# Optimization experiments

Measured on AMD Instinct MI355X. Metric: run time of the kernel, lower is better.

The kernel has to match this reference:

```python
import jax, jax.numpy as jnp
import numpy as np

H = 64       # HIDDEN_DIM
HIST = 4     # HIST_LEN
V = 64       # VOCAB_SIZE
LSTM_H = 32  # trigger LSTM hidden size


def setup_inputs() -> dict:
    key = jax.random.key(0)
    ks = jax.random.split(key, 24)
    B, L, M = 1024, 256, 256
    s = 0.1

    def p(k, shape):
        return jax.random.normal(k, shape, dtype=jnp.float32) * s

    return {
        "seq": jax.random.randint(ks[0], (B, L), 0, V, dtype=jnp.int32),
        "memory": jax.random.normal(ks[1], (B, M, H), dtype=jnp.float32),
        # nn.Embedding(V, H)
        "embed_w": p(ks[2], (V, H)),
        # nn.GRUCell(2H, H): weight_ih (3H, 2H), weight_hh (3H, H)
        "gru_wih": p(ks[3], (3 * H, 2 * H)),
        "gru_whh": p(ks[4], (3 * H, H)),
        "gru_bih": p(ks[5], (3 * H,)),
        "gru_bhh": p(ks[6], (3 * H,)),
        # SoftAttentionMemory projections: Linear(H, H) each
        "q_w": p(ks[7], (H, H)), "q_b": p(ks[8], (H,)),
        "k_w": p(ks[9], (H, H)), "k_b": p(ks[10], (H,)),
        "v_w": p(ks[11], (H, H)), "v_b": p(ks[12], (H,)),
        # PredictiveTrigger nn.LSTM(H, 32): gate order i,f,g,o
        "lstm_wih": p(ks[13], (4 * LSTM_H, H)),
        "lstm_whh": p(ks[14], (4 * LSTM_H, LSTM_H)),
        "lstm_bih": p(ks[15], (4 * LSTM_H,)),
        "lstm_bhh": p(ks[16], (4 * LSTM_H,)),
        "trig_w": p(ks[17], (1, LSTM_H)), "trig_b": p(ks[18], (1,)),
        # output head Linear(H, V)
        "head_w": p(ks[19], (V, H)), "head_b": p(ks[20], (V,)),
    }


def reference(seq, memory, embed_w, gru_wih, gru_whh, gru_bih, gru_bhh,
              q_w, q_b, k_w, k_b, v_w, v_b,
              lstm_wih, lstm_whh, lstm_bih, lstm_bhh,
              trig_w, trig_b, head_w, head_b):
    B, L = seq.shape
    x_emb = embed_w[seq]                         # (B, L, H)
    # k/v projections of memory are time-invariant -> hoist out of the loop
    kmem = memory @ k_w.T + k_b                  # (B, M, H)
    vmem = memory @ v_w.T + v_b                  # (B, M, H)
    scale = 1.0 / jnp.sqrt(jnp.float32(H))

    def gru_cell(inp, h):
        gi = inp @ gru_wih.T + gru_bih           # (B, 3H)
        gh = h @ gru_whh.T + gru_bhh
        i_r, i_z, i_n = jnp.split(gi, 3, axis=-1)
        h_r, h_z, h_n = jnp.split(gh, 3, axis=-1)
        r = jax.nn.sigmoid(i_r + h_r)
        z = jax.nn.sigmoid(i_z + h_z)
        n = jnp.tanh(i_n + r * h_n)
        return (1.0 - z) * n + z * h

    def trigger(hist):                            # hist: (B, HIST, H) -> (B,)
        def lstm_step(carry, x_t):
            hh, cc = carry
            g = x_t @ lstm_wih.T + lstm_bih + hh @ lstm_whh.T + lstm_bhh
            i, f, gg, o = jnp.split(g, 4, axis=-1)
            cc = jax.nn.sigmoid(f) * cc + jax.nn.sigmoid(i) * jnp.tanh(gg)
            hh = jax.nn.sigmoid(o) * jnp.tanh(cc)
            return (hh, cc), None
        init = (jnp.zeros((hist.shape[0], LSTM_H), hist.dtype),
                jnp.zeros((hist.shape[0], LSTM_H), hist.dtype))
        (hh, _), _ = jax.lax.scan(lstm_step, init, jnp.swapaxes(hist, 0, 1))
        return jax.nn.sigmoid(hh @ trig_w.T + trig_b)[:, 0]

    def attend(h):                                # (B, H) -> (B, H)
        q = h @ q_w.T + q_b
        w = jax.nn.softmax(jnp.einsum('bh,bmh->bm', q, kmem) * scale, axis=-1)
        return jnp.einsum('bm,bmh->bh', w, vmem)

    def step(carry, xs):
        h, retrieved, hist, reads = carry
        x_t, t = xs
        h = gru_cell(jnp.concatenate([x_t, retrieved], axis=-1), h)
        # torch uses h.detach() for the trigger history
        hist = jnp.concatenate([hist[:, 1:], jax.lax.stop_gradient(h)[:, None]], axis=1)
        full = t >= HIST - 1                      # history buffer filled
        prob = trigger(hist)
        do_read = full & (jnp.mean(prob) > 0.5)
        retrieved = jnp.where(do_read, attend(h),
                              jnp.where(full, jnp.zeros_like(retrieved), retrieved))
        reads = reads + do_read.astype(jnp.float32)
        return (h, retrieved, hist, reads), None

    carry0 = (jnp.zeros((B, H), jnp.float32),
              jnp.zeros((B, H), jnp.float32),
              jnp.zeros((B, HIST, H), jnp.float32),
              jnp.float32(0.0))
    (h, _, _, reads), _ = jax.lax.scan(step, carry0,
                                       (jnp.swapaxes(x_emb, 0, 1), jnp.arange(L)))
    logits = h @ head_w.T + head_b               # (B, V)
    read_rate = reads / L
    return logits, read_rate
```

## Files before the change

kernel.cpp:

```cpp
#include <hip/hip_runtime.h>
#include <hip/hip_fp16.h>
#include <math.h>

#define OFF_TOKPROJ 0
#define OFF_ACC     12288
#define OFF_SLOT2   12800
#define OFF_SLOTS   78336

#define THRESH30 (512ULL << 30)
#define THRESH27 (512ULL << 27)
#define SPIN_BOUND (1 << 18)

__device__ __forceinline__ float sigf(float x) {
    return __fdividef(1.f, 1.f + __expf(-x));
}
__device__ __forceinline__ float tanhf_fast(float x) {
    float e2 = __expf(-2.f * fabsf(x));
    float r = __fdividef(1.f - e2, 1.f + e2);
    return __uint_as_float(__float_as_uint(r) | (__float_as_uint(x) & 0x80000000u));
}
__device__ __forceinline__ float merged_go(float q, int l) {
    bool lo = (l < 32);
    float e = __expf(lo ? -2.f * fabsf(q) : -q);
    float m = __fdividef(lo ? (1.f - e) : 1.f, 1.f + e);
    if (lo) m = __uint_as_float(__float_as_uint(m) | (__float_as_uint(q) & 0x80000000u));
    return m;
}
__device__ __forceinline__ unsigned int pack2(float x, float y) {
    union { unsigned int u; _Float16 h[2]; } v;
    v.h[0] = (_Float16)x; v.h[1] = (_Float16)y;
    return v.u;
}
__device__ __forceinline__ float unplo(unsigned int u) {
    union { unsigned int x; _Float16 h[2]; } v; v.x = u; return (float)v.h[0];
}
__device__ __forceinline__ float unphi(unsigned int u) {
    union { unsigned int x; _Float16 h[2]; } v; v.x = u; return (float)v.h[1];
}
__device__ __forceinline__ float dot2acc(unsigned int a, unsigned int b, float acc) {
#if __has_builtin(__builtin_amdgcn_fdot2)
    typedef _Float16 hf2 __attribute__((ext_vector_type(2)));
    union { unsigned int u; hf2 h; } ua, ub;
    ua.u = a; ub.u = b;
    return __builtin_amdgcn_fdot2(ua.h, ub.h, acc, false);
#else
    union { unsigned int u; _Float16 h[2]; } ua, ub;
    ua.u = a; ub.u = b;
    return acc + (float)ua.h[0] * (float)ub.h[0] + (float)ua.h[1] * (float)ub.h[1];
#endif
}

__global__ __launch_bounds__(64) void prep_k(
    const float* __restrict__ embed, const float* __restrict__ gwih,
    const float* __restrict__ gbih, float* __restrict__ ws)
{
    int blk = blockIdx.x, l = threadIdx.x;
    if (blk < 64) {
        float* tokproj = ws + OFF_TOKPROJ;
        int v = blk;
        for (int j = l; j < 192; j += 64) {
            float s = gbih[j];
            for (int d = 0; d < 64; ++d) s += embed[v * 64 + d] * gwih[j * 128 + d];
            tokproj[v * 192 + j] = s;
        }
    } else {
        float* z = ws + OFF_SLOT2;
        int base = (blk - 64) * 4096;
        for (int i = base + l; i < base + 4096; i += 64) z[i] = 0.f;
    }
}

__global__ __launch_bounds__(256) void fused_k(
    const int* __restrict__ seq, const float* __restrict__ gwhh,
    const float* __restrict__ gbhh, const float* __restrict__ lwih,
    const float* __restrict__ lwhh, const float* __restrict__ lbih,
    const float* __restrict__ lbhh, const float* __restrict__ tw,
    const float* __restrict__ tb, const float* __restrict__ hw,
    const float* __restrict__ hb, float* __restrict__ ws,
    float* __restrict__ out)
{
    int tid = threadIdx.x, w = tid >> 6, l = tid & 63;
    int r = blockIdx.x;
    int gw = r & 3;
    const float* tokproj = ws + OFF_TOKPROJ;
    unsigned int* slots = (unsigned int*)(ws + OFF_SLOTS);

    __shared__ unsigned int hbuf[2][19][32];
    __shared__ unsigned int hs2w[4][16];
    __shared__ int toks[256];

    for (int i = tid; i < 256; i += 256) toks[i] = seq[(size_t)r * 256 + i];
    __syncthreads();

    if (w == gw) {
        unsigned int wh0h[32], wh1h[32], wh2h[32];
        #pragma unroll
        for (int d2 = 0; d2 < 32; ++d2) {
            wh0h[d2] = pack2(gwhh[(size_t)l * 64 + 2*d2], gwhh[(size_t)l * 64 + 2*d2 + 1]);
            wh1h[d2] = pack2(gwhh[(size_t)(64 + l) * 64 + 2*d2], gwhh[(size_t)(64 + l) * 64 + 2*d2 + 1]);
            wh2h[d2] = pack2(gwhh[(size_t)(128 + l) * 64 + 2*d2], gwhh[(size_t)(128 + l) * 64 + 2*d2 + 1]);
        }
        float g0b = gbhh[l], g1b = gbhh[64 + l], g2b = gbhh[128 + l];
        float h = 0.f;
        if (l < 32) { hbuf[0][0][l] = 0u; hbuf[0][1][l] = 0u; hbuf[0][2][l] = 0u; }
        int tok0 = toks[0];
        float gi0 = tokproj[tok0 * 192 + l], gi1 = tokproj[tok0 * 192 + 64 + l],
              gi2 = tokproj[tok0 * 192 + 128 + l];

        for (int c = 0; c < 16; ++c) {
            int cb = c & 1;
            if (c > 0 && l < 32) {
                hbuf[cb][0][l] = hbuf[cb ^ 1][16][l];
                hbuf[cb][1][l] = hbuf[cb ^ 1][17][l];
                hbuf[cb][2][l] = hbuf[cb ^ 1][18][l];
            }
            for (int s = 0; s < 16; ++s) {
                int t = c * 16 + s;
                float ni0 = 0.f, ni1 = 0.f, ni2 = 0.f;
                if (t < 255) {
                    int tk = toks[t + 1];
                    ni0 = tokproj[tk * 192 + l];
                    ni1 = tokproj[tk * 192 + 64 + l];
                    ni2 = tokproj[tk * 192 + 128 + l];
                }
                float A00 = 0.f, A01 = 0.f, A10 = 0.f, A11 = 0.f, A20 = 0.f, A21 = 0.f;
                #pragma unroll
                for (int d8 = 0; d8 < 8; ++d8) {
                    uint4 hv = *(const uint4*)&hbuf[cb][s + 2][d8 * 4];
                    A00 = dot2acc(hv.x, wh0h[d8*4+0], A00); A01 = dot2acc(hv.y, wh0h[d8*4+1], A01);
                    A00 = dot2acc(hv.z, wh0h[d8*4+2], A00); A01 = dot2acc(hv.w, wh0h[d8*4+3], A01);
                    A10 = dot2acc(hv.x, wh1h[d8*4+0], A10); A11 = dot2acc(hv.y, wh1h[d8*4+1], A11);
                    A10 = dot2acc(hv.z, wh1h[d8*4+2], A10); A11 = dot2acc(hv.w, wh1h[d8*4+3], A11);
                    A20 = dot2acc(hv.x, wh2h[d8*4+0], A20); A21 = dot2acc(hv.y, wh2h[d8*4+1], A21);
                    A20 = dot2acc(hv.z, wh2h[d8*4+2], A20); A21 = dot2acc(hv.w, wh2h[d8*4+3], A21);
                }
                float gh0 = g0b + A00 + A01;
                float gh1 = g1b + A10 + A11;
                float gh2 = g2b + A20 + A21;
                float r_ = sigf(gi0 + gh0), z_ = sigf(gi1 + gh1);
                float n_ = tanhf_fast(gi2 + r_ * gh2);
                h = (1.f - z_) * n_ + z_ * h;
                float a0 = __shfl(h, 2 * l), a1 = __shfl(h, 2 * l + 1);
                if (l < 32) hbuf[cb][s + 3][l] = pack2(a0, a1);
                gi0 = ni0; gi1 = ni1; gi2 = ni2;
            }
            __syncthreads();
        }
        float sL = hb[l];
        #pragma unroll
        for (int d4 = 0; d4 < 16; ++d4) {
            float4 w4 = *(const float4*)(hw + (size_t)l * 64 + d4 * 4);
            unsigned int h0 = hbuf[1][18][d4 * 2], h1 = hbuf[1][18][d4 * 2 + 1];
            sL += unplo(h0) * w4.x + unphi(h0) * w4.y + unplo(h1) * w4.z + unphi(h1) * w4.w;
        }
        out[r * 64 + l] = sL;
    } else {
        int tr = (w - gw + 3) & 3;
        unsigned int wl0h[32], wl1h[32], lh0h[16], lh1h[16];
        #pragma unroll
        for (int d2 = 0; d2 < 32; ++d2) {
            wl0h[d2] = pack2(lwih[(size_t)l * 64 + 2*d2], lwih[(size_t)l * 64 + 2*d2 + 1]);
            wl1h[d2] = pack2(lwih[(size_t)(64 + l) * 64 + 2*d2], lwih[(size_t)(64 + l) * 64 + 2*d2 + 1]);
        }
        #pragma unroll
        for (int d2 = 0; d2 < 16; ++d2) {
            lh0h[d2] = pack2(lwhh[(size_t)l * 32 + 2*d2], lwhh[(size_t)l * 32 + 2*d2 + 1]);
            lh1h[d2] = pack2(lwhh[(size_t)(64 + l) * 32 + 2*d2], lwhh[(size_t)(64 + l) * 32 + 2*d2 + 1]);
        }
        float lb0 = lbih[l] + lbhh[l], lb1 = lbih[64 + l] + lbhh[64 + l];
        float twr = (l < 32) ? tw[l] : 0.f;
        float tb0 = tb[0];

        auto do_chunk = [&](int cc) {
            int bb = cc & 1, base = cc * 16;
            int tlo = (cc == 0) ? 3 : base;
            int n = base + 16 - tlo;
            int ta = tlo + (tr * n) / 3;
            int tb_ = tlo + ((tr + 1) * n) / 3;
            auto proj = [&](int tt) -> unsigned int {
                int idx = tt - base + 3;
                float p0 = lb0, p1 = lb1;
                #pragma unroll
                for (int d8 = 0; d8 < 8; ++d8) {
                    uint4 hv = *(const uint4*)&hbuf[bb][idx][d8 * 4];
                    p0 = dot2acc(hv.x, wl0h[d8*4+0], p0); p1 = dot2acc(hv.x, wl1h[d8*4+0], p1);
                    p0 = dot2acc(hv.y, wl0h[d8*4+1], p0); p1 = dot2acc(hv.y, wl1h[d8*4+1], p1);
                    p0 = dot2acc(hv.z, wl0h[d8*4+2], p0); p1 = dot2acc(hv.z, wl1h[d8*4+2], p1);
                    p0 = dot2acc(hv.w, wl0h[d8*4+3], p0); p1 = dot2acc(hv.w, wl1h[d8*4+3], p1);
                }
                return pack2(p0, p1);
            };
            unsigned int PW[4];
            for (int t = ta; t < tb_; ++t) {
                if (t == ta) {
                    PW[0] = proj(t - 3); PW[1] = proj(t - 2);
                    PW[2] = proj(t - 1); PW[3] = proj(t);
                } else {
                    PW[0] = PW[1]; PW[1] = PW[2]; PW[2] = PW[3];
                    PW[3] = proj(t);
                }
                float hh = 0.f, cc2 = 0.f;
                #pragma unroll
                for (int k = 0; k < 4; ++k) {
                    float q0 = unplo(PW[k]), q1 = unphi(PW[k]);
                    if (k) {
                        #pragma unroll
                        for (int d4 = 0; d4 < 4; ++d4) {
                            uint4 ha = *(const uint4*)&hs2w[w][d4 * 4];
                            q0 = dot2acc(ha.x, lh0h[d4*4+0], q0); q1 = dot2acc(ha.x, lh1h[d4*4+0], q1);
                            q0 = dot2acc(ha.y, lh0h[d4*4+1], q0); q1 = dot2acc(ha.y, lh1h[d4*4+1], q1);
                            q0 = dot2acc(ha.z, lh0h[d4*4+2], q0); q1 = dot2acc(ha.z, lh1h[d4*4+2], q1);
                            q0 = dot2acc(ha.w, lh0h[d4*4+3], q0); q1 = dot2acc(ha.w, lh1h[d4*4+3], q1);
                        }
                    }
                    float s0 = sigf(q0);
                    float m  = merged_go(q1, l);
                    float ff = __shfl(s0, l + 32);
                    float oo = __shfl(m,  l + 32);
                    float ncc = ff * cc2 + s0 * m;
                    float nh = oo * tanhf_fast(ncc);
                    if (l < 32) { cc2 = ncc; hh = nh; }
                    if (k < 3) {
                        float a0 = __shfl(nh, 2 * l), a1 = __shfl(nh, 2 * l + 1);
                        if (l < 16) hs2w[w][l] = pack2(a0, a1);
                    }
                }
                float pp = (l < 32) ? hh * twr : 0.f;
                #pragma unroll
                for (int o = 32; o; o >>= 1) pp += __shfl_xor(pp, o);
                if (l == 0) {
                    float prob = sigf(pp + tb0);
                    unsigned long long q = (unsigned long long)llrint((double)prob * 1073741824.0);
                    if (q > 0x3FFFFFFFull) q = 0x3FFFFFFFull;
                    slots[(size_t)t * 1024 + r] = (unsigned int)q;
                }
            }
        };

        for (int c = 0; c < 16; ++c) {
            if (c > 0) do_chunk(c - 1);
            __syncthreads();
        }
        do_chunk(15);
    }
}

__global__ __launch_bounds__(256) void red_k(float* __restrict__ ws)
{
    int tid = threadIdx.x, w = tid >> 6, l = tid & 63;
    int t = 3 + blockIdx.x * 4 + w;
    if (t > 255) return;
    const unsigned int* slots = (const unsigned int*)(ws + OFF_SLOTS);
    unsigned long long* acc = (unsigned long long*)(ws + OFF_ACC);
    unsigned long long s = 0;
    #pragma unroll
    for (int k = 0; k < 16; ++k) s += slots[(size_t)t * 1024 + k * 64 + l];
    #pragma unroll
    for (int o = 32; o; o >>= 1) s += __shfl_xor(s, o);
    if (l == 0) acc[t] = s;
}

__global__ __launch_bounds__(256, 1) void fin_k(
    const int* __restrict__ seq, const float* __restrict__ memory,
    const float* __restrict__ gwih, const float* __restrict__ gwhh,
    const float* __restrict__ gbhh, const float* __restrict__ qw,
    const float* __restrict__ qb, const float* __restrict__ kw,
    const float* __restrict__ vw, const float* __restrict__ vb,
    const float* __restrict__ lwih, const float* __restrict__ lwhh,
    const float* __restrict__ lbih, const float* __restrict__ lbhh,
    const float* __restrict__ tw, const float* __restrict__ tb,
    const float* __restrict__ hw, const float* __restrict__ hb,
    float* __restrict__ ws, float* __restrict__ out)
{
    int tid = threadIdx.x, w = tid >> 6, l = tid & 63, b = blockIdx.x;
    const unsigned long long* acc = (const unsigned long long*)(ws + OFF_ACC);

    __shared__ int redmin[4];
    {
        int mymin = 1 << 30;
        if (tid >= 3 && acc[tid] > THRESH30) mymin = tid;
        #pragma unroll
        for (int o = 32; o; o >>= 1) mymin = min(mymin, __shfl_xor(mymin, o));
        if (l == 0) redmin[w] = mymin;
    }
    __syncthreads();
    int tc = min(min(redmin[0], redmin[1]), min(redmin[2], redmin[3]));
    if (tc > 255) {
        if (b == 0 && tid == 0) out[65536] = 0.f;
        return;
    }

    int r = b * 4 + w;
    const float* tokproj = ws + OFF_TOKPROJ;
    unsigned int* S2 = (unsigned int*)(ws + OFF_SLOT2);

    __shared__ float hs[4][64], qs[4][64], us[4][64], rs[4][64];
    __shared__ float hs2f[4][32];
    __shared__ float PXl[4][4][128];
    __shared__ unsigned int probq[4];
    __shared__ int flagLds;
    __shared__ int toks[4][256];

    for (int k = 0; k < 4; ++k) toks[w][k * 64 + l] = seq[r * 256 + k * 64 + l];
    if (tid == 0) flagLds = 0;

    float wh0[64], wh1[64], wh2[64], wl0[64], wl1[64], lh0[32], lh1[32];
    #pragma unroll
    for (int d4 = 0; d4 < 16; ++d4) {
        float4 a0 = *(const float4*)(gwhh + (size_t)l * 64 + d4 * 4);
        float4 a1 = *(const float4*)(gwhh + (size_t)(64 + l) * 64 + d4 * 4);
        float4 a2 = *(const float4*)(gwhh + (size_t)(128 + l) * 64 + d4 * 4);
        float4 b0 = *(const float4*)(lwih + (size_t)l * 64 + d4 * 4);
        float4 b1 = *(const float4*)(lwih + (size_t)(64 + l) * 64 + d4 * 4);
        wh0[d4*4] = a0.x; wh0[d4*4+1] = a0.y; wh0[d4*4+2] = a0.z; wh0[d4*4+3] = a0.w;
        wh1[d4*4] = a1.x; wh1[d4*4+1] = a1.y; wh1[d4*4+2] = a1.z; wh1[d4*4+3] = a1.w;
        wh2[d4*4] = a2.x; wh2[d4*4+1] = a2.y; wh2[d4*4+2] = a2.z; wh2[d4*4+3] = a2.w;
        wl0[d4*4] = b0.x; wl0[d4*4+1] = b0.y; wl0[d4*4+2] = b0.z; wl0[d4*4+3] = b0.w;
        wl1[d4*4] = b1.x; wl1[d4*4+1] = b1.y; wl1[d4*4+2] = b1.z; wl1[d4*4+3] = b1.w;
    }
    #pragma unroll
    for (int d4 = 0; d4 < 8; ++d4) {
        float4 c0 = *(const float4*)(lwhh + (size_t)l * 32 + d4 * 4);
        float4 c1 = *(const float4*)(lwhh + (size_t)(64 + l) * 32 + d4 * 4);
        lh0[d4*4] = c0.x; lh0[d4*4+1] = c0.y; lh0[d4*4+2] = c0.z; lh0[d4*4+3] = c0.w;
        lh1[d4*4] = c1.x; lh1[d4*4+1] = c1.y; lh1[d4*4+2] = c1.z; lh1[d4*4+3] = c1.w;
    }
    float g0b = gbhh[l], g1b = gbhh[64 + l], g2b = gbhh[128 + l];
    float lb0 = lbih[l] + lbhh[l], lb1 = lbih[64 + l] + lbhh[64 + l];
    float twr = (l < 32) ? tw[l] : 0.f;
    float tb0 = tb[0];
    const float* mrow = memory + (size_t)r * 16384;

    float h = 0.f;
    hs[w][l] = 0.f;
    bool fire = false, brk = false;
    int cnt = 1;
    __syncthreads();

    for (int t = 0; t < 256; ++t) {
        int tok = toks[w][t];
        float gi0 = tokproj[tok * 192 + l], gi1 = tokproj[tok * 192 + 64 + l],
              gi2 = tokproj[tok * 192 + 128 + l];
        float gh0 = g0b, gh1 = g1b, gh2 = g2b;
        #pragma unroll
        for (int d4 = 0; d4 < 16; ++d4) {
            float4 hv = *(const float4*)&hs[w][d4 * 4];
            gh0 += hv.x*wh0[d4*4] + hv.y*wh0[d4*4+1] + hv.z*wh0[d4*4+2] + hv.w*wh0[d4*4+3];
            gh1 += hv.x*wh1[d4*4] + hv.y*wh1[d4*4+1] + hv.z*wh1[d4*4+2] + hv.w*wh1[d4*4+3];
            gh2 += hv.x*wh2[d4*4] + hv.y*wh2[d4*4+1] + hv.z*wh2[d4*4+2] + hv.w*wh2[d4*4+3];
        }
        if (fire) {
            float q = qb[l];
            #pragma unroll
            for (int d4 = 0; d4 < 16; ++d4) {
                float4 q4 = *(const float4*)(qw + (size_t)l * 64 + d4 * 4);
                float4 hv = *(const float4*)&hs[w][d4 * 4];
                q += hv.x * q4.x + hv.y * q4.y + hv.z * q4.z + hv.w * q4.w;
            }
            qs[w][l] = q;
            float qk = 0.f;
            for (int e = 0; e < 64; ++e) qk += qs[w][e] * kw[(size_t)e * 64 + l];
            qk *= 0.125f;
            us[w][l] = qk;
            float sc[4];
            for (int k = 0; k < 4; ++k) {
                const float* mp = mrow + (size_t)(k * 64 + l) * 64;
                float s = 0.f;
                #pragma unroll
                for (int d4 = 0; d4 < 16; ++d4) {
                    float4 m4 = *(const float4*)(mp + d4 * 4);
                    float4 kv = *(const float4*)&us[w][d4 * 4];
                    s += m4.x * kv.x + m4.y * kv.y + m4.z * kv.z + m4.w * kv.w;
                }
                sc[k] = s;
            }
            float mx = fmaxf(fmaxf(sc[0], sc[1]), fmaxf(sc[2], sc[3]));
            for (int o = 32; o; o >>= 1) mx = fmaxf(mx, __shfl_xor(mx, o));
            float den = 0.f;
            #pragma unroll
            for (int k = 0; k < 4; ++k) { sc[k] = expf(sc[k] - mx); den += sc[k]; }
            for (int o = 32; o; o >>= 1) den += __shfl_xor(den, o);
            float u = 0.f;
            for (int m = 0; m < 256; ++m) {
                float wm = __shfl(sc[m >> 6], m & 63);
                u += wm * mrow[(size_t)m * 64 + l];
            }
            u /= den;
            us[w][l] = u;
            float ret = vb[l];
            #pragma unroll
            for (int d4 = 0; d4 < 16; ++d4) {
                float4 v4 = *(const float4*)(vw + (size_t)l * 64 + d4 * 4);
                float4 uv = *(const float4*)&us[w][d4 * 4];
                ret += uv.x * v4.x + uv.y * v4.y + uv.z * v4.z + uv.w * v4.w;
            }
            rs[w][l] = ret;
            for (int e = 0; e < 64; ++e) {
                float re = rs[w][e];
                gi0 += re * gwih[(size_t)l * 128 + 64 + e];
                gi1 += re * gwih[(size_t)(64 + l) * 128 + 64 + e];
                gi2 += re * gwih[(size_t)(128 + l) * 128 + 64 + e];
            }
        }
        fire = false;
        float r_ = sigf(gi0 + gh0), z_ = sigf(gi1 + gh1);
        float n_ = tanhf_fast(gi2 + r_ * gh2);
        h = (1.f - z_) * n_ + z_ * h;
        hs[w][l] = h;

        float p0 = lb0, p1 = lb1;
        #pragma unroll
        for (int d4 = 0; d4 < 16; ++d4) {
            float4 hv = *(const float4*)&hs[w][d4 * 4];
            p0 += hv.x*wl0[d4*4] + hv.y*wl0[d4*4+1] + hv.z*wl0[d4*4+2] + hv.w*wl0[d4*4+3];
            p1 += hv.x*wl1[d4*4] + hv.y*wl1[d4*4+1] + hv.z*wl1[d4*4+2] + hv.w*wl1[d4*4+3];
        }
        PXl[w][t & 3][l] = p0; PXl[w][t & 3][64 + l] = p1;

        if (t == tc) {
            fire = true;
        } else if (t > tc) {
            float hh = 0.f, cc = 0.f;
            #pragma unroll
            for (int k = 0; k < 4; ++k) {
                int s2 = (t - 3 + k) & 3;
                float q0 = PXl[w][s2][l], q1 = PXl[w][s2][64 + l];
                if (k) {
                    #pragma unroll
                    for (int d4 = 0; d4 < 8; ++d4) {
                        float4 hv = *(const float4*)&hs2f[w][d4 * 4];
                        q0 += hv.x*lh0[d4*4] + hv.y*lh0[d4*4+1] + hv.z*lh0[d4*4+2] + hv.w*lh0[d4*4+3];
                        q1 += hv.x*lh1[d4*4] + hv.y*lh1[d4*4+1] + hv.z*lh1[d4*4+2] + hv.w*lh1[d4*4+3];
                    }
                }
                float f_ = __shfl(q0, l + 32), o_ = __shfl(q1, l + 32);
                float ig = sigf(q0), ff = sigf(f_), gg = tanhf_fast(q1), oo = sigf(o_);
                float ncc = ff * cc + ig * gg;
                float nhh = oo * tanhf_fast(ncc);
                if (l < 32) { cc = ncc; hh = nhh; hs2f[w][l] = nhh; }
            }
            float pp = (l < 32) ? hh * twr : 0.f;
            #pragma unroll
            for (int o = 32; o; o >>= 1) pp += __shfl_xor(pp, o);
            if (l == 0) {
                float prob = sigf(pp + tb0);
                unsigned long long q = (unsigned long long)llrint((double)prob * 134217728.0);
                if (q > 0x7FFFFFFull) q = 0x7FFFFFFull;
                probq[w] = (unsigned int)q;
            }
            __syncthreads();
            if (w == 0 && l == 0) {
                unsigned int s = probq[0] + probq[1] + probq[2] + probq[3];
                __hip_atomic_store(&S2[(size_t)t * 256 + b], (1u << 30) | s,
                                   __ATOMIC_RELAXED, __HIP_MEMORY_SCOPE_AGENT);
            }
            if (w == 0) {
                unsigned long long tot = 0; int spin = 0; bool ok = true;
                if (!brk) {
                    for (;;) {
                        bool all4 = true; tot = 0;
                        #pragma unroll
                        for (int k2 = 0; k2 < 4; ++k2) {
                            unsigned int v = __hip_atomic_load(&S2[(size_t)t * 256 + k2 * 64 + l],
                                                               __ATOMIC_RELAXED, __HIP_MEMORY_SCOPE_AGENT);
                            all4 &= ((v >> 30) == 1u);
                            tot += (v & 0x3FFFFFFFu);
                        }
                        if (__all(all4)) break;
                        if (++spin > SPIN_BOUND) { ok = false; brk = true; break; }
                        __builtin_amdgcn_s_sleep(1);
                    }
                } else ok = false;
                #pragma unroll
                for (int o = 32; o; o >>= 1) tot += __shfl_xor(tot, o);
                int dec = (ok && tot > THRESH27) ? 1 : 0;
                cnt += dec;
                if (l == 0) flagLds = dec;
            }
            __syncthreads();
            fire = (flagLds != 0);
        }
    }

    float sL = hb[l];
    #pragma unroll
    for (int d4 = 0; d4 < 16; ++d4) {
        float4 w4 = *(const float4*)(hw + (size_t)l * 64 + d4 * 4);
        float4 hv = *(const float4*)&hs[w][d4 * 4];
        sL += hv.x * w4.x + hv.y * w4.y + hv.z * w4.z + hv.w * w4.w;
    }
    out[r * 64 + l] = sL;
    if (b == 0 && w == 0 && l == 0)
        out[65536] = brk ? -1234.f : (float)cnt / 256.f;
}

extern "C" void kernel_launch(void* const* d_in, const int* in_sizes, int n_in,
                              void* d_out, int out_size, void* d_ws, size_t ws_size,
                              hipStream_t stream)
{
    const int*   seq    = (const int*)d_in[0];
    const float* memory = (const float*)d_in[1];
    const float* embed  = (const float*)d_in[2];
    const float* gwih   = (const float*)d_in[3];
    const float* gwhh   = (const float*)d_in[4];
    const float* gbih   = (const float*)d_in[5];
    const float* gbhh   = (const float*)d_in[6];
    const float* qw     = (const float*)d_in[7];
    const float* qb     = (const float*)d_in[8];
    const float* kw     = (const float*)d_in[9];
    const float* vw     = (const float*)d_in[11];
    const float* vb     = (const float*)d_in[12];
    const float* lwih   = (const float*)d_in[13];
    const float* lwhh   = (const float*)d_in[14];
    const float* lbih   = (const float*)d_in[15];
    const float* lbhh   = (const float*)d_in[16];
    const float* tw     = (const float*)d_in[17];
    const float* tb     = (const float*)d_in[18];
    const float* hw     = (const float*)d_in[19];
    const float* hb     = (const float*)d_in[20];
    float* ws = (float*)d_ws;
    float* out = (float*)d_out;

    prep_k<<<80, 64, 0, stream>>>(embed, gwih, gbih, ws);
    fused_k<<<1024, 256, 0, stream>>>(seq, gwhh, gbhh, lwih, lwhh, lbih, lbhh,
                                      tw, tb, hw, hb, ws, out);
    red_k<<<64, 256, 0, stream>>>(ws);
    fin_k<<<256, 256, 0, stream>>>(seq, memory, gwih, gwhh, gbhh, qw, qb, kw,
                                   vw, vb, lwih, lwhh, lbih, lbhh, tw, tb,
                                   hw, hb, ws, out);
}
```

Before: 456.6 us.

## Process two batch rows per block in fused GRU/trigger kernel

Each fused_k block now advances two independent sequences, so 512 blocks replace 1024. The GRU warp interleaves the two rows' recurrent dot products to expose ILP and hide the latency of the serial step chain. The three trigger warps split the combined 2×chunk work among themselves. This roughly doubles the per-step work in the GRU warp and its register pressure, and halves the grid, which may lower occupancy and parallelism across CUs.

```diff
diff --git a/kernel.cpp b/kernel.cpp
--- a/kernel.cpp
+++ b/kernel.cpp
@@ -80,16 +80,16 @@
     float* __restrict__ out)
 {
     int tid = threadIdx.x, w = tid >> 6, l = tid & 63;
-    int r = blockIdx.x;
-    int gw = r & 3;
+    int b = blockIdx.x;
+    int gw = b & 3;
     const float* tokproj = ws + OFF_TOKPROJ;
     unsigned int* slots = (unsigned int*)(ws + OFF_SLOTS);
 
-    __shared__ unsigned int hbuf[2][19][32];
+    __shared__ unsigned int hbuf[2][2][19][32];
     __shared__ unsigned int hs2w[4][16];
-    __shared__ int toks[256];
-
-    for (int i = tid; i < 256; i += 256) toks[i] = seq[(size_t)r * 256 + i];
+    __shared__ int toks[2][256];
+
+    for (int i = tid; i < 512; i += 256) toks[i >> 8][i & 255] = seq[(size_t)b * 512 + i];
     __syncthreads();
 
     if (w == gw) {
@@ -101,59 +101,88 @@
             wh2h[d2] = pack2(gwhh[(size_t)(128 + l) * 64 + 2*d2], gwhh[(size_t)(128 + l) * 64 + 2*d2 + 1]);
         }
         float g0b = gbhh[l], g1b = gbhh[64 + l], g2b = gbhh[128 + l];
-        float h = 0.f;
-        if (l < 32) { hbuf[0][0][l] = 0u; hbuf[0][1][l] = 0u; hbuf[0][2][l] = 0u; }
-        int tok0 = toks[0];
-        float gi0 = tokproj[tok0 * 192 + l], gi1 = tokproj[tok0 * 192 + 64 + l],
-              gi2 = tokproj[tok0 * 192 + 128 + l];
+        float h0 = 0.f, h1 = 0.f;
+        if (l < 32) {
+            hbuf[0][0][0][l] = 0u; hbuf[0][0][1][l] = 0u; hbuf[0][0][2][l] = 0u;
+            hbuf[1][0][0][l] = 0u; hbuf[1][0][1][l] = 0u; hbuf[1][0][2][l] = 0u;
+        }
+        int ta = toks[0][0], tbk = toks[1][0];
+        float ga0 = tokproj[ta * 192 + l], ga1 = tokproj[ta * 192 + 64 + l],
+              ga2 = tokproj[ta * 192 + 128 + l];
+        float gb0 = tokproj[tbk * 192 + l], gb1 = tokproj[tbk * 192 + 64 + l],
+              gb2 = tokproj[tbk * 192 + 128 + l];
 
         for (int c = 0; c < 16; ++c) {
             int cb = c & 1;
             if (c > 0 && l < 32) {
-                hbuf[cb][0][l] = hbuf[cb ^ 1][16][l];
-                hbuf[cb][1][l] = hbuf[cb ^ 1][17][l];
-                hbuf[cb][2][l] = hbuf[cb ^ 1][18][l];
+                hbuf[0][cb][0][l] = hbuf[0][cb ^ 1][16][l];
+                hbuf[0][cb][1][l] = hbuf[0][cb ^ 1][17][l];
+                hbuf[0][cb][2][l] = hbuf[0][cb ^ 1][18][l];
+                hbuf[1][cb][0][l] = hbuf[1][cb ^ 1][16][l];
+                hbuf[1][cb][1][l] = hbuf[1][cb ^ 1][17][l];
+                hbuf[1][cb][2][l] = hbuf[1][cb ^ 1][18][l];
             }
             for (int s = 0; s < 16; ++s) {
                 int t = c * 16 + s;
-                float ni0 = 0.f, ni1 = 0.f, ni2 = 0.f;
+                float na0 = 0.f, na1 = 0.f, na2 = 0.f, nb0 = 0.f, nb1 = 0.f, nb2 = 0.f;
                 if (t < 255) {
-                    int tk = toks[t + 1];
-                    ni0 = tokproj[tk * 192 + l];
-                    ni1 = tokproj[tk * 192 + 64 + l];
-                    ni2 = tokproj[tk * 192 + 128 + l];
+                    int tk0 = toks[0][t + 1], tk1 = toks[1][t + 1];
+                    na0 = tokproj[tk0 * 192 + l];
+                    na1 = tokproj[tk0 * 192 + 64 + l];
+                    na2 = tokproj[tk0 * 192 + 128 + l];
+                    nb0 = tokproj[tk1 * 192 + l];
+                    nb1 = tokproj[tk1 * 192 + 64 + l];
+                    nb2 = tokproj[tk1 * 192 + 128 + l];
                 }
-                float A00 = 0.f, A01 = 0.f, A10 = 0.f, A11 = 0.f, A20 = 0.f, A21 = 0.f;
+                float A00=0.f, A01=0.f, A10=0.f, A11=0.f, A20=0.f, A21=0.f;
+                float B00=0.f, B01=0.f, B10=0.f, B11=0.f, B20=0.f, B21=0.f;
                 #pragma unroll
                 for (int d8 = 0; d8 < 8; ++d8) {
-                    uint4 hv = *(const uint4*)&hbuf[cb][s + 2][d8 * 4];
-                    A00 = dot2acc(hv.x, wh0h[d8*4+0], A00); A01 = dot2acc(hv.y, wh0h[d8*4+1], A01);
-                    A00 = dot2acc(hv.z, wh0h[d8*4+2], A00); A01 = dot2acc(hv.w, wh0h[d8*4+3], A01);
-                    A10 = dot2acc(hv.x, wh1h[d8*4+0], A10); A11 = dot2acc(hv.y, wh1h[d8*4+1], A11);
-                    A10 = dot2acc(hv.z, wh1h[d8*4+2], A10); A11 = dot2acc(hv.w, wh1h[d8*4+3], A11);
-                    A20 = dot2acc(hv.x, wh2h[d8*4+0], A20); A21 = dot2acc(hv.y, wh2h[d8*4+1], A21);
-                    A20 = dot2acc(hv.z, wh2h[d8*4+2], A20); A21 = dot2acc(hv.w, wh2h[d8*4+3], A21);
+                    uint4 hv0 = *(const uint4*)&hbuf[0][cb][s + 2][d8 * 4];
+                    uint4 hv1 = *(const uint4*)&hbuf[1][cb][s + 2][d8 * 4];
+                    A00 = dot2acc(hv0.x, wh0h[d8*4+0], A00); A01 = dot2acc(hv0.y, wh0h[d8*4+1], A01);
+                    B00 = dot2acc(hv1.x, wh0h[d8*4+0], B00); B01 = dot2acc(hv1.y, wh0h[d8*4+1], B01);
+                    A00 = dot2acc(hv0.z, wh0h[d8*4+2], A00); A01 = dot2acc(hv0.w, wh0h[d8*4+3], A01);
+                    B00 = dot2acc(hv1.z, wh0h[d8*4+2], B00); B01 = dot2acc(hv1.w, wh0h[d8*4+3], B01);
+                    A10 = dot2acc(hv0.x, wh1h[d8*4+0], A10); A11 = dot2acc(hv0.y, wh1h[d8*4+1], A11);
+                    B10 = dot2acc(hv1.x, wh1h[d8*4+0], B10); B11 = dot2acc(hv1.y, wh1h[d8*4+1], B11);
+                    A10 = dot2acc(hv0.z, wh1h[d8*4+2], A10); A11 = dot2acc(hv0.w, wh1h[d8*4+3], A11);
+                    B10 = dot2acc(hv1.z, wh1h[d8*4+2], B10); B11 = dot2acc(hv1.w, wh1h[d8*4+3], B11);
+                    A20 = dot2acc(hv0.x, wh2h[d8*4+0], A20); A21 = dot2acc(hv0.y, wh2h[d8*4+1], A21);
+                    B20 = dot2acc(hv1.x, wh2h[d8*4+0], B20); B21 = dot2acc(hv1.y, wh2h[d8*4+1], B21);
+                    A20 = dot2acc(hv0.z, wh2h[d8*4+2], A20); A21 = dot2acc(hv0.w, wh2h[d8*4+3], A21);
+                    B20 = dot2acc(hv1.z, wh2h[d8*4+2], B20); B21 = dot2acc(hv1.w, wh2h[d8*4+3], B21);
                 }
-                float gh0 = g0b + A00 + A01;
-                float gh1 = g1b + A10 + A11;
-                float gh2 = g2b + A20 + A21;
-                float r_ = sigf(gi0 + gh0), z_ = sigf(gi1 + gh1);
-                float n_ = tanhf_fast(gi2 + r_ * gh2);
-                h = (1.f - z_) * n_ + z_ * h;
-                float a0 = __shfl(h, 2 * l), a1 = __shfl(h, 2 * l + 1);
-                if (l < 32) hbuf[cb][s + 3][l] = pack2(a0, a1);
-                gi0 = ni0; gi1 = ni1; gi2 = ni2;
+                float r0_ = sigf(ga0 + g0b + A00 + A01);
+                float r1_ = sigf(gb0 + g0b + B00 + B01);
+                float z0_ = sigf(ga1 + g1b + A10 + A11);
+                float z1_ = sigf(gb1 + g1b + B10 + B11);
+                float n0_ = tanhf_fast(ga2 + r0_ * (g2b + A20 + A21));
+                float n1_ = tanhf_fast(gb2 + r1_ * (g2b + B20 + B21));
+                h0 = (1.f - z0_) * n0_ + z0_ * h0;
+                h1 = (1.f - z1_) * n1_ + z1_ * h1;
+                float a0 = __shfl(h0, 2 * l), a1 = __shfl(h0, 2 * l + 1);
+                float b0 = __shfl(h1, 2 * l), b1 = __shfl(h1, 2 * l + 1);
+                if (l < 32) {
+                    hbuf[0][cb][s + 3][l] = pack2(a0, a1);
+                    hbuf[1][cb][s + 3][l] = pack2(b0, b1);
+                }
+                ga0 = na0; ga1 = na1; ga2 = na2;
+                gb0 = nb0; gb1 = nb1; gb2 = nb2;
             }
             __syncthreads();
         }
-        float sL = hb[l];
-        #pragma unroll
-        for (int d4 = 0; d4 < 16; ++d4) {
-            float4 w4 = *(const float4*)(hw + (size_t)l * 64 + d4 * 4);
-            unsigned int h0 = hbuf[1][18][d4 * 2], h1 = hbuf[1][18][d4 * 2 + 1];
-            sL += unplo(h0) * w4.x + unphi(h0) * w4.y + unplo(h1) * w4.z + unphi(h1) * w4.w;
-        }
-        out[r * 64 + l] = sL;
+        #pragma unroll
+        for (int row = 0; row < 2; ++row) {
+            float sL = hb[l];
+            #pragma unroll
+            for (int d4 = 0; d4 < 16; ++d4) {
+                float4 w4 = *(const float4*)(hw + (size_t)l * 64 + d4 * 4);
+                unsigned int q0 = hbuf[row][1][18][d4 * 2], q1 = hbuf[row][1][18][d4 * 2 + 1];
+                sL += unplo(q0) * w4.x + unphi(q0) * w4.y + unplo(q1) * w4.z + unphi(q1) * w4.w;
+            }
+            out[(size_t)(b * 2 + row) * 64 + l] = sL;
+        }
     } else {
         int tr = (w - gw + 3) & 3;
         unsigned int wl0h[32], wl1h[32], lh0h[16], lh1h[16];
@@ -175,65 +204,72 @@
             int bb = cc & 1, base = cc * 16;
             int tlo = (cc == 0) ? 3 : base;
             int n = base + 16 - tlo;
-            int ta = tlo + (tr * n) / 3;
-            int tb_ = tlo + ((tr + 1) * n) / 3;
-            auto proj = [&](int tt) -> unsigned int {
-                int idx = tt - base + 3;
-                float p0 = lb0, p1 = lb1;
-                #pragma unroll
-                for (int d8 = 0; d8 < 8; ++d8) {
-                    uint4 hv = *(const uint4*)&hbuf[bb][idx][d8 * 4];
-                    p0 = dot2acc(hv.x, wl0h[d8*4+0], p0); p1 = dot2acc(hv.x, wl1h[d8*4+0], p1);
-                    p0 = dot2acc(hv.y, wl0h[d8*4+1], p0); p1 = dot2acc(hv.y, wl1h[d8*4+1], p1);
-                    p0 = dot2acc(hv.z, wl0h[d8*4+2], p0); p1 = dot2acc(hv.z, wl1h[d8*4+2], p1);
-                    p0 = dot2acc(hv.w, wl0h[d8*4+3], p0); p1 = dot2acc(hv.w, wl1h[d8*4+3], p1);
-                }
-                return pack2(p0, p1);
-            };
-            unsigned int PW[4];
-            for (int t = ta; t < tb_; ++t) {
-                if (t == ta) {
-                    PW[0] = proj(t - 3); PW[1] = proj(t - 2);
-                    PW[2] = proj(t - 1); PW[3] = proj(t);
-                } else {
-                    PW[0] = PW[1]; PW[1] = PW[2]; PW[2] = PW[3];
-                    PW[3] = proj(t);
-                }
-                float hh = 0.f, cc2 = 0.f;
-                #pragma unroll
-                for (int k = 0; k < 4; ++k) {
-                    float q0 = unplo(PW[k]), q1 = unphi(PW[k]);
-                    if (k) {
-                        #pragma unroll
-                        for (int d4 = 0; d4 < 4; ++d4) {
-                            uint4 ha = *(const uint4*)&hs2w[w][d4 * 4];
-                            q0 = dot2acc(ha.x, lh0h[d4*4+0], q0); q1 = dot2acc(ha.x, lh1h[d4*4+0], q1);
-                            q0 = dot2acc(ha.y, lh0h[d4*4+1], q0); q1 = dot2acc(ha.y, lh1h[d4*4+1], q1);
-                            q0 = dot2acc(ha.z, lh0h[d4*4+2], q0); q1 = dot2acc(ha.z, lh1h[d4*4+2], q1);
-                            q0 = dot2acc(ha.w, lh0h[d4*4+3], q0); q1 = dot2acc(ha.w, lh1h[d4*4+3], q1);
+            int total = 2 * n;
+            int i0 = (tr * total) / 3, i1 = ((tr + 1) * total) / 3;
+            int i = i0;
+            while (i < i1) {
+                int row = i / n;
+                int tstart = tlo + (i - row * n);
+                int iend = min(i1, (row + 1) * n);
+                int tend = tlo + (iend - row * n);
+                auto proj = [&](int tt) -> unsigned int {
+                    int idx = tt - base + 3;
+                    float p0 = lb0, p1 = lb1;
+                    #pragma unroll
+                    for (int d8 = 0; d8 < 8; ++d8) {
+                        uint4 hv = *(const uint4*)&hbuf[row][bb][idx][d8 * 4];
+                        p0 = dot2acc(hv.x, wl0h[d8*4+0], p0); p1 = dot2acc(hv.x, wl1h[d8*4+0], p1);
+                        p0 = dot2acc(hv.y, wl0h[d8*4+1], p0); p1 = dot2acc(hv.y, wl1h[d8*4+1], p1);
+                        p0 = dot2acc(hv.z, wl0h[d8*4+2], p0); p1 = dot2acc(hv.z, wl1h[d8*4+2], p1);
+                        p0 = dot2acc(hv.w, wl0h[d8*4+3], p0); p1 = dot2acc(hv.w, wl1h[d8*4+3], p1);
+                    }
+                    return pack2(p0, p1);
+                };
+                unsigned int PW[4];
+                PW[0] = proj(tstart - 3); PW[1] = proj(tstart - 2);
+                PW[2] = proj(tstart - 1); PW[3] = proj(tstart);
+                for (int t = tstart; t < tend; ++t) {
+                    if (t > tstart) {
+                        PW[0] = PW[1]; PW[1] = PW[2]; PW[2] = PW[3];
+                        PW[3] = proj(t);
+                    }
+                    float hh = 0.f, cc2 = 0.f;
+                    #pragma unroll
+                    for (int k = 0; k < 4; ++k) {
+                        float q0 = unplo(PW[k]), q1 = unphi(PW[k]);
+                        if (k) {
+                            #pragma unroll
+                            for (int d4 = 0; d4 < 4; ++d4) {
+                                uint4 ha = *(const uint4*)&hs2w[w][d4 * 4];
+                                q0 = dot2acc(ha.x, lh0h[d4*4+0], q0); q1 = dot2acc(ha.x, lh1h[d4*4+0], q1);
+                                q0 = dot2acc(ha.y, lh0h[d4*4+1], q0); q1 = dot2acc(ha.y, lh1h[d4*4+1], q1);
+                                q0 = dot2acc(ha.z, lh0h[d4*4+2], q0); q1 = dot2acc(ha.z, lh1h[d4*4+2], q1);
+                                q0 = dot2acc(ha.w, lh0h[d4*4+3], q0); q1 = dot2acc(ha.w, lh1h[d4*4+3], q1);
+                            }
+                        }
+                        float s0 = sigf(q0);
+                        float m  = merged_go(q1, l);
+                        float ff = __shfl(s0, l + 32);
+                        float oo = __shfl(m,  l + 32);
+                        float ncc = ff * cc2 + s0 * m;
+                        float nh = oo * tanhf_fast(ncc);
+                        if (l < 32) { cc2 = ncc; hh = nh; }
+                        if (k < 3) {
+                            float a0 = __shfl(nh, 2 * l), a1 = __shfl(nh, 2 * l + 1);
+                            if (l < 16) hs2w[w][l] = pack2(a0, a1);
                         }
                     }
-                    float s0 = sigf(q0);
-                    float m  = merged_go(q1, l);
-                    float ff = __shfl(s0, l + 32);
-                    float oo = __shfl(m,  l + 32);
-                    float ncc = ff * cc2 + s0 * m;
-                    float nh = oo * tanhf_fast(ncc);
-                    if (l < 32) { cc2 = ncc; hh = nh; }
-                    if (k < 3) {
-                        float a0 = __shfl(nh, 2 * l), a1 = __shfl(nh, 2 * l + 1);
-                        if (l < 16) hs2w[w][l] = pack2(a0, a1);
+                    float pp = (l < 32) ? hh * twr : 0.f;
+                    #pragma unroll
+                    for (int o = 32; o; o >>= 1) pp += __shfl_xor(pp, o);
+                    if (l == 0) {
+                        float prob = sigf(pp + tb0);
+                        unsigned long long q = (unsigned long long)llrint((double)prob * 1073741824.0);
+                        if (q > 0x3FFFFFFFull) q = 0x3FFFFFFFull;
+                        slots[(size_t)t * 1024 + (b * 2 + row)] = (unsigned int)q;
                     }
                 }
-                float pp = (l < 32) ? hh * twr : 0.f;
-                #pragma unroll
-                for (int o = 32; o; o >>= 1) pp += __shfl_xor(pp, o);
-                if (l == 0) {
-                    float prob = sigf(pp + tb0);
-                    unsigned long long q = (unsigned long long)llrint((double)prob * 1073741824.0);
-                    if (q > 0x3FFFFFFFull) q = 0x3FFFFFFFull;
-                    slots[(size_t)t * 1024 + r] = (unsigned int)q;
-                }
+                i = iend;
             }
         };
 
@@ -522,8 +558,8 @@
     float* out = (float*)d_out;
 
     prep_k<<<80, 64, 0, stream>>>(embed, gwih, gbih, ws);
-    fused_k<<<1024, 256, 0, stream>>>(seq, gwhh, gbhh, lwih, lwhh, lbih, lbhh,
-                                      tw, tb, hw, hb, ws, out);
+    fused_k<<<512, 256, 0, stream>>>(seq, gwhh, gbhh, lwih, lwhh, lbih, lbhh,
+                                     tw, tb, hw, hb, ws, out);
     red_k<<<64, 256, 0, stream>>>(ws);
     fin_k<<<256, 256, 0, stream>>>(seq, memory, gwih, gwhh, gbhh, qw, qb, kw,
                                    vw, vb, lwih, lwhh, lbih, lbhh, tw, tb,
```

After: 441.9 us. -3.2%, faster.
